# Optimization experiments

Hardware: AMD Instinct MI355X
Metric: run time of the kernel (lower is better)

## Reference

```python
import jax, jax.numpy as jnp
import numpy as np

FS = 16000
NUM_BANDS = 15
CENTER_FREQ = 150
FFT_SIZE = 512
FFT_IN = 256
HOP = 128
NUM_FRAMES = 30
BETA = 1.0 + 10.0 ** (15.0 / 20.0)
FFT_PAD = (FFT_SIZE - FFT_IN) // 2
ROWS = FFT_SIZE // 2 + 1


def _make_fftmat():
    window = np.hanning(FFT_IN)
    window = np.concatenate([np.zeros(FFT_PAD), window, np.zeros(FFT_PAD)])
    fft = np.fft.fft(np.eye(FFT_SIZE))
    fft = np.vstack((np.real(fft[:ROWS, :]), np.imag(fft[:ROWS, :])))
    fft = window * fft  # (2*ROWS, FFT_SIZE)
    return fft.astype(np.float32)


def _make_octmat(fs=FS, nfft=FFT_SIZE, numBands=NUM_BANDS, mn=CENTER_FREQ):
    f = np.linspace(0, fs, nfft + 1)
    f = f[: int(nfft / 2) + 1]
    k = np.arange(float(numBands))
    cf = 2 ** (k / 3) * mn
    fl = np.sqrt(2.0 ** (k / 3) * mn * 2 ** ((k - 1.0) / 3) * mn)
    fr = np.sqrt(2.0 ** (k / 3) * mn * 2 ** ((k + 1.0) / 3) * mn)
    A = np.zeros((numBands, len(f)))
    for i in range(len(cf)):
        b = np.argmin((f - fl[i]) ** 2)
        fl[i] = f[b]
        fl_ii = b
        b = np.argmin((f - fr[i]) ** 2)
        fr[i] = f[b]
        fr_ii = b
        A[i, np.arange(fl_ii, fr_ii)] = 1
    rnk = np.sum(A, axis=1)
    nb = np.where((rnk[1:] >= rnk[:-1]) & (rnk[1:] != 0))[-1][-1] + 1
    A = A[: nb + 1, :]
    return A.astype(np.float32)


def setup_inputs() -> dict:
    key = jax.random.key(0)
    k1, k2, k3 = jax.random.split(key, 3)
    B, L = 64, 128000
    return {
        "prediction": jax.random.normal(k1, (B, L), dtype=jnp.float32),
        "target": jax.random.normal(k2, (B, L), dtype=jnp.float32),
        "inteference": jax.random.normal(k3, (B, L), dtype=jnp.float32),
        "fftmat": jnp.asarray(_make_fftmat()),   # (514, 512)
        "octmat": jnp.asarray(_make_octmat()),   # (n_bands, 257)
    }


def _stft_mag(seq, fftmat):
    # seq: (B, L) -> conv1d with stride HOP, padding FFT_PAD
    out = jax.lax.conv_general_dilated(
        seq[:, None, :], fftmat[:, None, :],
        window_strides=(HOP,), padding=[(FFT_PAD, FFT_PAD)],
        dimension_numbers=("NCH", "OIH", "NCH"))
    real, imag = out[:, :ROWS, :], out[:, ROWS:, :]
    return jnp.sqrt(real ** 2 + imag ** 2)  # (B, ROWS, T)


def _stoi_loss(prediction, target, fftmat, octmat):
    pred_mag = _stft_mag(prediction, fftmat)
    targ_mag = _stft_mag(target, fftmat)
    # octave-band energies: (B, n_bands, T)
    x = jnp.sqrt(jnp.einsum("bft,kf->bkt", targ_mag ** 2, octmat))
    y = jnp.sqrt(jnp.einsum("bft,kf->bkt", pred_mag ** 2, octmat))
    T = x.shape[2]
    W = T - NUM_FRAMES  # windows for m in [NUM_FRAMES, T)
    idx = jnp.arange(W)[:, None] + jnp.arange(NUM_FRAMES)[None, :]  # (W, 30)
    xw = x[:, :, idx]  # (B, K, W, 30)
    yw = y[:, :, idx]
    alpha = jnp.sqrt(jnp.sum(xw ** 2, axis=3, keepdims=True)
                     / (jnp.sum(yw ** 2, axis=3, keepdims=True) + 1e-07))
    yp = jnp.minimum(alpha * yw, BETA * xw)
    xn = xw - jnp.mean(xw, axis=3, keepdims=True)
    xn = xn / jnp.sqrt(jnp.sum(xn ** 2, axis=3, keepdims=True))
    yn = yp - jnp.mean(yp, axis=3, keepdims=True)
    yn = yn / jnp.sqrt(jnp.sum(yn ** 2, axis=3, keepdims=True))
    # per-window correlation: mean over (B, K) of sum over time
    r = jnp.mean(jnp.sum(xn * yn, axis=3), axis=(0, 1))  # (W,)
    return -jnp.sum(r) / W


def reference(prediction, target, inteference, fftmat, octmat):
    return _stoi_loss(prediction, target, fftmat, octmat)
```

## Files before the change

kernel.cpp:

```cpp
#include <hip/hip_runtime.h>
#include <math.h>

#define SIG_L 128000
#define NBATCH 64
#define NROWS 257
#define HOP 128
#define NUMF 999
#define NFRM 30
#define NWIN 969
#define NB_MAX 16
#define FBINS 160
#define TILES 9
#define KSTEPS 16
#define FPBX 256
#define AKB 18432
#define BCH 4112
#define SMEMSZ (2 * AKB + BCH * 16 + NB_MAX * FPBX * 4 + 640)
#define BETA_F 6.623413251903491f

typedef __attribute__((ext_vector_type(8))) short short8;
typedef __attribute__((ext_vector_type(16))) float f32x16;
typedef unsigned short ushort_t;

__device__ inline ushort_t bf_hi_rne(float v, float* rem) {
    unsigned u = __float_as_uint(v);
    unsigned hr = (u + 0x7FFFu + ((u >> 16) & 1u)) & 0xFFFF0000u;
    *rem = v - __uint_as_float(hr);
    return (ushort_t)(hr >> 16);
}
__device__ inline ushort_t bf_rne(float v) {
    unsigned u = __float_as_uint(v);
    return (ushort_t)((u + 0x7FFFu + ((u >> 16) & 1u)) >> 16);
}

__device__ inline void gll16(const void* g, void* l) {
    __builtin_amdgcn_global_load_lds(
        (const __attribute__((address_space(1))) unsigned int*)g,
        (__attribute__((address_space(3))) unsigned int*)l, 16, 0, 0);
}

__global__ void k_scan(const float* __restrict__ oct, int NB, int* __restrict__ hdr) {
    __shared__ int smin[16], smax[16];
    int tid = threadIdx.x;
    if (tid < NB) { smin[tid] = 0x7fffffff; smax[tid] = -1; }
    __syncthreads();
    for (int idx = tid; idx < NB * NROWS; idx += blockDim.x) {
        int k = idx / NROWS, f = idx % NROWS;
        if (oct[idx] != 0.0f) { atomicMin(&smin[k], f); atomicMax(&smax[k], f); }
    }
    __syncthreads();
    if (tid < FBINS) {
        int kid = -1;
        for (int k = 0; k < NB; ++k)
            if (smax[k] >= 0 && tid >= smin[k] && tid <= smax[k]) kid = k;
        hdr[32 + tid] = kid;
    }
}

__global__ void k_prep(const float* __restrict__ fftmat, ushort_t* __restrict__ wpack) {
    for (int u = 0; u < 2; ++u) {
        int idx = blockIdx.x * 512 + u * 256 + threadIdx.x;
        int e = idx & 7, l = (idx >> 3) & 63, p = (idx >> 9) & 1;
        int tt = (idx >> 10) % TILES, kk = (idx >> 10) / TILES;
        int row32 = l & 31, kq = l >> 5;
        int bin = tt * 16 + (row32 >> 1);
        int part = row32 & 1;
        int k = kk * 16 + kq * 8 + e;
        float v = fftmat[(size_t)(part ? (NROWS + bin) : bin) * 512 + 128 + k];
        float rem; ushort_t hb = bf_hi_rne(v, &rem);
        wpack[idx] = p ? bf_rne(rem) : hb;
    }
}

__global__ __launch_bounds__(768, 3) void k_probe(float* sink) {
    __shared__ __align__(16) char smem[SMEMSZ];
    float* bacc = (float*)smem;
    const int tid = threadIdx.x;
    for (int i = tid; i < 4096; i += 768) bacc[i] = 0.0f;
    __syncthreads();
    float v = bacc[(tid * 37 + 1) & 4095];
    asm volatile("" :: "v"(v));
    (void)sink;
}

__global__ __launch_bounds__(768, 3) void k_stft(
    const float* __restrict__ targ, const float* __restrict__ pred,
    const ushort_t* __restrict__ wpack, const int* __restrict__ hdr,
    float* __restrict__ xbuf, float* __restrict__ ybuf, int NB) {
    __shared__ __align__(16) char smem[SMEMSZ];
    ushort_t* As    = (ushort_t*)smem;
    char*     Bs    = smem + 2 * AKB;
    float*    bacc  = (float*)(smem + 2 * AKB + BCH * 16);
    int*      kmapS = (int*)(smem + 2 * AKB + BCH * 16 + NB_MAX * FPBX * 4);

    const int tid = threadIdx.x;
    const int lane = tid & 63;
    const int wv = __builtin_amdgcn_readfirstlane(tid >> 6);
    const int mg  = wv >> 2;
    const int col = wv & 3;
    const int tbase = mg * 3;
    const int jloc = lane & 31, kq = lane >> 5;

    for (int i = tid; i < FBINS; i += 768) kmapS[i] = hdr[32 + i];

#pragma unroll 1
    for (int task = 0; task < 2; ++task) {
        const int t = (int)blockIdx.x + 256 * task;
        const int z = t & 1, b = (t >> 1) & 63, tile = (t >> 7) & 3;
        const int t0 = tile * FPBX;
        const float* __restrict__ sig = z ? pred : targ;
        float* __restrict__ out = z ? ybuf : xbuf;
        const size_t boff = (size_t)b * SIG_L;

        if (task) __syncthreads();
        for (int i = tid; i < NB_MAX * FPBX; i += 768) bacc[i] = 0.0f;

        const long sbase = (long)t0 * HOP;
        float4 xr[12];
#pragma unroll
        for (int u = 0; u < 6; ++u) {
            const int c = tid + u * 768;
            const long g0 = sbase + (long)c * 8;
            const bool full = (c < BCH) && (g0 + 8 <= SIG_L);
            const long gc = full ? g0 : 0;
            const float* p = sig + boff + gc;
            float4 a0 = *(const float4*)(p);
            float4 a1 = *(const float4*)(p + 4);
            if (!full) { a0 = (float4){0,0,0,0}; a1 = (float4){0,0,0,0}; }
            xr[2*u] = a0; xr[2*u+1] = a1;
        }
#pragma unroll
        for (int u = 0; u < 6; ++u) {
            const int c = tid + u * 768;
            if (c < BCH) {
                short8 sv;
                sv[0]=(short)bf_rne(xr[2*u].x);   sv[1]=(short)bf_rne(xr[2*u].y);
                sv[2]=(short)bf_rne(xr[2*u].z);   sv[3]=(short)bf_rne(xr[2*u].w);
                sv[4]=(short)bf_rne(xr[2*u+1].x); sv[5]=(short)bf_rne(xr[2*u+1].y);
                sv[6]=(short)bf_rne(xr[2*u+1].z); sv[7]=(short)bf_rne(xr[2*u+1].w);
                int byte = c * 16;
                byte ^= ((byte >> 8) & 0xF) << 4;
                *(short8*)(Bs + byte) = sv;
            }
        }
        {
            const char* gsrc = (const char*)wpack;
            for (int j = wv; j < 18; j += 12)
                gll16(gsrc + j * 1024 + lane * 16, smem + j * 1024);
        }
        __syncthreads();

        f32x16 acc[3][2];
#pragma unroll
        for (int g = 0; g < 3; ++g)
#pragma unroll
            for (int bt = 0; bt < 2; ++bt)
#pragma unroll
                for (int e = 0; e < 16; ++e) acc[g][bt][e] = 0.0f;

        int cur = 0;
#pragma unroll 1
        for (int kk = 0; kk < KSTEPS; ++kk) {
            if (kk < KSTEPS - 1) {
                const char* gsrc = (const char*)wpack + (size_t)(kk + 1) * AKB;
                char* ldst = smem + (cur ^ 1) * AKB;
                for (int j = wv; j < 18; j += 12)
                    gll16(gsrc + j * 1024 + lane * 16, ldst + j * 1024);
            }
            short8 S[2];
#pragma unroll
            for (int bt = 0; bt < 2; ++bt) {
                const int fl = col * 64 + bt * 32 + jloc;
                int byte = fl * 256 + kk * 32 + kq * 16;
                byte ^= ((byte >> 8) & 0xF) << 4;
                S[bt] = *(const short8*)(Bs + byte);
            }
            const ushort_t* ab = As + cur * (AKB / 2) + tbase * 1024 + lane * 8;
            __builtin_amdgcn_s_setprio(1);
#pragma unroll
            for (int g = 0; g < 3; ++g) {
                short8 Ah = *(const short8*)(ab + g * 1024);
                short8 Al = *(const short8*)(ab + g * 1024 + 512);
                acc[g][0] = __builtin_amdgcn_mfma_f32_32x32x16_bf16(Ah, S[0], acc[g][0], 0, 0, 0);
                acc[g][1] = __builtin_amdgcn_mfma_f32_32x32x16_bf16(Ah, S[1], acc[g][1], 0, 0, 0);
                acc[g][0] = __builtin_amdgcn_mfma_f32_32x32x16_bf16(Al, S[0], acc[g][0], 0, 0, 0);
                acc[g][1] = __builtin_amdgcn_mfma_f32_32x32x16_bf16(Al, S[1], acc[g][1], 0, 0, 0);
            }
            __builtin_amdgcn_s_setprio(0);
            __syncthreads();
            cur ^= 1;
        }

#pragma unroll
        for (int g = 0; g < 3; ++g) {
#pragma unroll
            for (int bt = 0; bt < 2; ++bt) {
                const int fl = col * 64 + bt * 32 + jloc;
                float run = 0.0f; int runk = -1;
#pragma unroll
                for (int rr = 0; rr < 8; ++rr) {
                    const int m = (rr & 1) + 4 * (rr >> 1) + 2 * kq;
                    const int kid = kmapS[(tbase + g) * 16 + m];
                    const float vr = acc[g][bt][rr * 2], vi = acc[g][bt][rr * 2 + 1];
                    const float e = vr * vr + vi * vi;
                    if (kid != runk) {
                        if (runk >= 0) atomicAdd(&bacc[runk * FPBX + fl], run);
                        run = 0.0f; runk = kid;
                    }
                    if (kid >= 0) run += e;
                }
                if (runk >= 0) atomicAdd(&bacc[runk * FPBX + fl], run);
            }
        }
        __syncthreads();
        for (int idx = tid; idx < NB * FPBX; idx += 768) {
            int k = idx >> 8, tt = idx & (FPBX - 1);
            int tg = t0 + tt;
            if (tg < NUMF)
                out[((size_t)b * NB + k) * NUMF + tg] = bacc[k * FPBX + tt];
        }
    }
}

__global__ __launch_bounds__(256) void k_corr(const float* __restrict__ xbuf,
                                              const float* __restrict__ ybuf,
                                              int NB, double* __restrict__ partials) {
    const int k = blockIdx.x, b = blockIdx.y;
    const long roff = ((long)b * NB + k) * NUMF;
    __shared__ float xl[NUMF], yl[NUMF];
    __shared__ double red[256];
    const int tid = threadIdx.x;
    for (int i = tid; i < NUMF; i += 256) {
        xl[i] = sqrtf(xbuf[roff + i]);
        yl[i] = sqrtf(ybuf[roff + i]);
    }
    __syncthreads();
    double loc = 0.0;
    for (int w = tid; w < NWIN; w += 256) {
        float sx = 0, sxx = 0, syy = 0;
        for (int i = 0; i < NFRM; ++i) {
            float xv = xl[w + i], yv = yl[w + i];
            sx += xv; sxx += xv * xv; syy += yv * yv;
        }
        float alpha = sqrtf(sxx / (syy + 1e-7f));
        float sy = 0;
        for (int i = 0; i < NFRM; ++i)
            sy += fminf(alpha * yl[w + i], BETA_F * xl[w + i]);
        float mx = sx * (1.0f / NFRM), my = sy * (1.0f / NFRM);
        float cxx = 0, cyy = 0, cxy = 0;
        for (int i = 0; i < NFRM; ++i) {
            float dx = xl[w + i] - mx;
            float dy = fminf(alpha * yl[w + i], BETA_F * xl[w + i]) - my;
            cxx += dx * dx; cyy += dy * dy; cxy += dx * dy;
        }
        loc += (double)cxy / sqrt((double)cxx * (double)cyy);
    }
    red[tid] = loc;
    __syncthreads();
    for (int s = 128; s > 0; s >>= 1) {
        if (tid < s) red[tid] += red[tid + s];
        __syncthreads();
    }
    if (tid == 0) partials[b * NB + k] = red[0];
}

__global__ void k_final(const double* __restrict__ partials, int NB, float* __restrict__ out) {
    __shared__ double red[256];
    const int tid = threadIdx.x;
    const int n = NBATCH * NB;
    double s = 0.0;
    for (int i = tid; i < n; i += 256) s += partials[i];
    red[tid] = s;
    __syncthreads();
    for (int st = 128; st > 0; st >>= 1) {
        if (tid < st) red[tid] += red[tid + st];
        __syncthreads();
    }
    if (tid == 0) out[0] = (float)(-red[0] / ((double)NBATCH * NB * NWIN));
}

extern "C" void kernel_launch(void* const* d_in, const int* in_sizes, int n_in,
                              void* d_out, int out_size, void* d_ws, size_t ws_size,
                              hipStream_t stream) {
    const float* pred   = (const float*)d_in[0];
    const float* targ   = (const float*)d_in[1];
    const float* fftmat = (const float*)d_in[3];
    const float* oct    = (const float*)d_in[4];
    const int NB = in_sizes[4] / NROWS;

    char* ws = (char*)d_ws;
    int*      hdr   = (int*)ws;
    ushort_t* wpack = (ushort_t*)(ws + 1024);
    size_t o1 = 1024 + (size_t)KSTEPS * TILES * 2 * 512 * 2;
    size_t xsz = (size_t)NBATCH * NB_MAX * NUMF * 4;
    float*  xbuf = (float*)(ws + o1);
    float*  ybuf = (float*)(ws + o1 + xsz);
    double* partials = (double*)(ws + o1 + 2 * xsz);

    hipLaunchKernelGGL(k_scan, dim3(1), dim3(256), 0, stream, oct, NB, hdr);
    hipLaunchKernelGGL(k_prep, dim3(288), dim3(256), 0, stream, fftmat, wpack);
    hipLaunchKernelGGL(k_probe, dim3(512), dim3(768), 0, stream, xbuf);
    hipLaunchKernelGGL(k_stft, dim3(256), dim3(768), 0, stream,
                       targ, pred, wpack, hdr, xbuf, ybuf, NB);
    hipLaunchKernelGGL(k_corr, dim3(NB, NBATCH), dim3(256), 0, stream, xbuf, ybuf, NB, partials);
    hipLaunchKernelGGL(k_final, dim3(1), dim3(256), 0, stream, partials, NB, (float*)d_out);
}
```

Before: 105.7 us.

## Merge setup kernels, drop probe kernel, register-block correlation windows

Merges the octave-band scan and weight-packing kernels into one launch and removes the dummy probe kernel, which cuts two kernel launches and their gaps. The correlation kernel now gives each thread four consecutive windows and loads the 33 samples they share into registers, so it no longer re-reads shared memory for each window. The cost is higher register pressure in the correlation kernel. The probe kernel may have been warming the LDS or clocks, so dropping it could change the timing of the STFT kernel.

Result: faster. 99.07 us (median of 2 runs) (-6.2%).

```diff
diff --git a/kernel.cpp b/kernel.cpp
--- a/kernel.cpp
+++ b/kernel.cpp
@@ -39,27 +39,29 @@
         (__attribute__((address_space(3))) unsigned int*)l, 16, 0, 0);
 }
 
-__global__ void k_scan(const float* __restrict__ oct, int NB, int* __restrict__ hdr) {
-    __shared__ int smin[16], smax[16];
-    int tid = threadIdx.x;
-    if (tid < NB) { smin[tid] = 0x7fffffff; smax[tid] = -1; }
-    __syncthreads();
-    for (int idx = tid; idx < NB * NROWS; idx += blockDim.x) {
-        int k = idx / NROWS, f = idx % NROWS;
-        if (oct[idx] != 0.0f) { atomicMin(&smin[k], f); atomicMax(&smax[k], f); }
-    }
-    __syncthreads();
-    if (tid < FBINS) {
-        int kid = -1;
-        for (int k = 0; k < NB; ++k)
-            if (smax[k] >= 0 && tid >= smin[k] && tid <= smax[k]) kid = k;
-        hdr[32 + tid] = kid;
-    }
-}
-
-__global__ void k_prep(const float* __restrict__ fftmat, ushort_t* __restrict__ wpack) {
+__global__ void k_setup(const float* __restrict__ oct, const float* __restrict__ fftmat,
+                        int NB, int* __restrict__ hdr, ushort_t* __restrict__ wpack) {
+    const int tid = threadIdx.x;
+    if (blockIdx.x == 0) {
+        __shared__ int smin[16], smax[16];
+        if (tid < NB) { smin[tid] = 0x7fffffff; smax[tid] = -1; }
+        __syncthreads();
+        for (int idx = tid; idx < NB * NROWS; idx += blockDim.x) {
+            int k = idx / NROWS, f = idx % NROWS;
+            if (oct[idx] != 0.0f) { atomicMin(&smin[k], f); atomicMax(&smax[k], f); }
+        }
+        __syncthreads();
+        if (tid < FBINS) {
+            int kid = -1;
+            for (int k = 0; k < NB; ++k)
+                if (smax[k] >= 0 && tid >= smin[k] && tid <= smax[k]) kid = k;
+            hdr[32 + tid] = kid;
+        }
+        return;
+    }
+    const int bx = blockIdx.x - 1;
     for (int u = 0; u < 2; ++u) {
-        int idx = blockIdx.x * 512 + u * 256 + threadIdx.x;
+        int idx = bx * 512 + u * 256 + tid;
         int e = idx & 7, l = (idx >> 3) & 63, p = (idx >> 9) & 1;
         int tt = (idx >> 10) % TILES, kk = (idx >> 10) / TILES;
         int row32 = l & 31, kq = l >> 5;
@@ -70,17 +72,6 @@
         float rem; ushort_t hb = bf_hi_rne(v, &rem);
         wpack[idx] = p ? bf_rne(rem) : hb;
     }
-}
-
-__global__ __launch_bounds__(768, 3) void k_probe(float* sink) {
-    __shared__ __align__(16) char smem[SMEMSZ];
-    float* bacc = (float*)smem;
-    const int tid = threadIdx.x;
-    for (int i = tid; i < 4096; i += 768) bacc[i] = 0.0f;
-    __syncthreads();
-    float v = bacc[(tid * 37 + 1) & 4095];
-    asm volatile("" :: "v"(v));
-    (void)sink;
 }
 
 __global__ __launch_bounds__(768, 3) void k_stft(
@@ -235,25 +226,40 @@
         yl[i] = sqrtf(ybuf[roff + i]);
     }
     __syncthreads();
+
+    const int w0 = tid * 4;
+    float xr[33], yr[33];
+#pragma unroll
+    for (int i = 0; i < 33; ++i) {
+        int idx = w0 + i; idx = (idx < NUMF) ? idx : (NUMF - 1);
+        xr[i] = xl[idx]; yr[i] = yl[idx];
+    }
     double loc = 0.0;
-    for (int w = tid; w < NWIN; w += 256) {
-        float sx = 0, sxx = 0, syy = 0;
-        for (int i = 0; i < NFRM; ++i) {
-            float xv = xl[w + i], yv = yl[w + i];
-            sx += xv; sxx += xv * xv; syy += yv * yv;
-        }
-        float alpha = sqrtf(sxx / (syy + 1e-7f));
-        float sy = 0;
-        for (int i = 0; i < NFRM; ++i)
-            sy += fminf(alpha * yl[w + i], BETA_F * xl[w + i]);
-        float mx = sx * (1.0f / NFRM), my = sy * (1.0f / NFRM);
-        float cxx = 0, cyy = 0, cxy = 0;
-        for (int i = 0; i < NFRM; ++i) {
-            float dx = xl[w + i] - mx;
-            float dy = fminf(alpha * yl[w + i], BETA_F * xl[w + i]) - my;
-            cxx += dx * dx; cyy += dy * dy; cxy += dx * dy;
-        }
-        loc += (double)cxy / sqrt((double)cxx * (double)cyy);
+#pragma unroll
+    for (int j = 0; j < 4; ++j) {
+        const int w = w0 + j;
+        if (w < NWIN) {
+            float sx = 0, sxx = 0, syy = 0;
+#pragma unroll
+            for (int i = 0; i < NFRM; ++i) {
+                float xv = xr[j + i], yv = yr[j + i];
+                sx += xv; sxx += xv * xv; syy += yv * yv;
+            }
+            float alpha = sqrtf(sxx / (syy + 1e-7f));
+            float sy = 0;
+#pragma unroll
+            for (int i = 0; i < NFRM; ++i)
+                sy += fminf(alpha * yr[j + i], BETA_F * xr[j + i]);
+            float mx = sx * (1.0f / NFRM), my = sy * (1.0f / NFRM);
+            float cxx = 0, cyy = 0, cxy = 0;
+#pragma unroll
+            for (int i = 0; i < NFRM; ++i) {
+                float dx = xr[j + i] - mx;
+                float dy = fminf(alpha * yr[j + i], BETA_F * xr[j + i]) - my;
+                cxx += dx * dx; cyy += dy * dy; cxy += dx * dy;
+            }
+            loc += (double)cxy / sqrt((double)cxx * (double)cyy);
+        }
     }
     red[tid] = loc;
     __syncthreads();
@@ -297,9 +303,7 @@
     float*  ybuf = (float*)(ws + o1 + xsz);
     double* partials = (double*)(ws + o1 + 2 * xsz);
 
-    hipLaunchKernelGGL(k_scan, dim3(1), dim3(256), 0, stream, oct, NB, hdr);
-    hipLaunchKernelGGL(k_prep, dim3(288), dim3(256), 0, stream, fftmat, wpack);
-    hipLaunchKernelGGL(k_probe, dim3(512), dim3(768), 0, stream, xbuf);
+    hipLaunchKernelGGL(k_setup, dim3(289), dim3(256), 0, stream, oct, fftmat, NB, hdr, wpack);
     hipLaunchKernelGGL(k_stft, dim3(256), dim3(768), 0, stream,
                        targ, pred, wpack, hdr, xbuf, ybuf, NB);
     hipLaunchKernelGGL(k_corr, dim3(NB, NBATCH), dim3(256), 0, stream, xbuf, ybuf, NB, partials);
```
